# Kernel optimization log

Hardware: AMD Instinct MI355X
Metric: run time of the kernel (lower is better)

The kernel has to match this reference:

```python
import jax, jax.numpy as jnp
import numpy as np
from jax import lax

C, H, W = 256, 56, 56
KP, STRIDE = 9, 2
M_CH, D, T = 64, 128, 16
TOPK = 32
SIGMA, ALPHA, TAU, EPS = 3.0, 10.0, 10.0, 1e-6
B = 4
N = H * W
PAD = KP // 2


def _build_M_P(h, w, s):
    ys = np.arange(0, h, s)
    xs = np.arange(0, w, s)
    ny, nx = len(ys), len(xs)
    N_, K_ = h * w, ny * nx
    by, bx = np.meshgrid(np.arange(h, dtype=np.float32), np.arange(w, dtype=np.float32), indexing='ij')
    bx = bx.reshape(-1)
    by = by.reshape(-1)
    fx, fy = bx / float(s), by / float(s)
    x0 = np.floor(fx).astype(np.int64)
    y0 = np.floor(fy).astype(np.int64)
    x0c = np.clip(x0, 0, nx - 1)
    x1c = np.clip(x0 + 1, 0, nx - 1)
    y0c = np.clip(y0, 0, ny - 1)
    y1c = np.clip(y0 + 1, 0, ny - 1)
    wx = fx - x0
    wy = fy - y0
    Mm = np.zeros((N_, K_), dtype=np.float32)
    rows = np.arange(N_)
    Mm[rows, y0c * nx + x0c] += (1 - wx) * (1 - wy)
    Mm[rows, y0c * nx + x1c] += wx * (1 - wy)
    Mm[rows, y1c * nx + x0c] += (1 - wx) * wy
    Mm[rows, y1c * nx + x1c] += wx * wy
    rs = Mm.sum(1, keepdims=True)
    rs[rs == 0] = 1.0
    Mm = Mm / rs
    P = np.stack([bx, by], axis=-1).astype(np.float32)  # (N,2) (x,y)
    return Mm, P


def _forward(feature_map, A_bank, pw_w, pw_b, proj_w, proj_b, r, M, P):
    def make_grid(A):  # affine_grid, align_corners=False
        xs = (2.0 * jnp.arange(W, dtype=jnp.float32) + 1.0) / W - 1.0
        ys = (2.0 * jnp.arange(H, dtype=jnp.float32) + 1.0) / H - 1.0
        gy, gx = jnp.meshgrid(ys, xs, indexing='ij')
        base = jnp.stack([gx, gy, jnp.ones_like(gx)], axis=-1)  # (H,W,3)
        return base @ A.T  # (H,W,2) normalized (x,y)

    def grid_sample(grid):  # bilinear, border padding, align_corners=False
        ix = ((grid[..., 0] + 1.0) * W - 1.0) / 2.0
        iy = ((grid[..., 1] + 1.0) * H - 1.0) / 2.0
        x0 = jnp.floor(ix)
        y0 = jnp.floor(iy)
        wx = ix - x0
        wy = iy - y0
        x0c = jnp.clip(x0, 0, W - 1).astype(jnp.int32)
        x1c = jnp.clip(x0 + 1, 0, W - 1).astype(jnp.int32)
        y0c = jnp.clip(y0, 0, H - 1).astype(jnp.int32)
        y1c = jnp.clip(y0 + 1, 0, H - 1).astype(jnp.int32)
        fm = feature_map.reshape(B, C, H * W)
        def g(yc, xc):
            return fm[:, :, (yc * W + xc).reshape(-1)].reshape(B, C, H, W)
        return (g(y0c, x0c) * (1 - wx) * (1 - wy) + g(y0c, x1c) * wx * (1 - wy)
                + g(y1c, x0c) * (1 - wx) * wy + g(y1c, x1c) * wx * wy)

    grids = jax.vmap(make_grid)(A_bank)          # (T,H,W,2)
    warped = jax.vmap(grid_sample)(grids)        # (T,B,C,H,W)

    # unfold(k,pad,stride) -> 1x1 conv -> spatial mean  ==  zero-padded avg-pool then linear
    pm = lax.reduce_window(warped, 0.0, lax.add,
                           (1, 1, 1, KP, KP), (1, 1, 1, STRIDE, STRIDE),
                           [(0, 0), (0, 0), (0, 0), (PAD, PAD), (PAD, PAD)]) / (KP * KP)
    Tn, Bn, Cn, Kh, Kw = pm.shape
    K = Kh * Kw
    pm = pm.reshape(Tn, Bn, Cn, K).transpose(0, 1, 3, 2)  # (T,B,K,C)
    x = pm @ pw_w.T + pw_b                                 # (T,B,K,m)
    z = x @ proj_w.T + proj_b                              # (T,B,K,d)
    z = z / jnp.maximum(jnp.linalg.norm(z, axis=-1, keepdims=True), EPS)
    Z = z.transpose(1, 0, 2, 3)                            # (B,T,K,d)

    s = jnp.einsum('btkd,d->btk', Z, r)
    wgt = jax.nn.softmax(TAU * s, axis=1)[..., None]
    g_emb = jnp.sum(wgt * Z, axis=1)                       # (B,K,d)

    E = jnp.einsum('nk,bkd->bnd', M, g_emb)
    E = E / jnp.maximum(jnp.linalg.norm(E, axis=-1, keepdims=True), EPS)

    d2 = jnp.sum((P[:, None, :] - P[None, :, :]) ** 2, axis=-1)  # (N,N)
    G = 1.0 - jnp.exp(-d2 / (2.0 * SIGMA ** 2))
    Saff = jnp.einsum('bnd,bmd->bnm', E, E) * G

    vals, idx = lax.top_k(Saff, TOPK)
    bidx = jnp.arange(B)[:, None, None]
    nidx = jnp.arange(N)[None, :, None]
    S_sp = jnp.zeros_like(Saff).at[bidx, nidx, idx].set(vals)
    A0 = jax.nn.softmax(ALPHA * S_sp, axis=-1) * jax.nn.softmax(ALPHA * S_sp, axis=-2)
    return E, A0


def setup_inputs() -> dict:
    key = jax.random.key(0)
    ks = jax.random.split(key, 6)
    feature_map = jax.random.normal(ks[0], (B, C, H, W), jnp.float32)
    ident = jnp.broadcast_to(jnp.array([[1.0, 0.0, 0.0], [0.0, 1.0, 0.0]], jnp.float32), (T, 2, 3))
    A_bank = ident + 0.1 * jax.random.normal(ks[1], (T, 2, 3), jnp.float32)
    pw_w = jax.random.normal(ks[2], (M_CH, C), jnp.float32) / np.sqrt(C).astype(np.float32)
    pw_b = jnp.zeros((M_CH,), jnp.float32)
    proj_w = jax.random.normal(ks[3], (D, M_CH), jnp.float32) / np.sqrt(M_CH).astype(np.float32)
    proj_b = jnp.zeros((D,), jnp.float32)
    r = 0.01 * jax.random.normal(ks[4], (D,), jnp.float32)
    Mnp, Pnp = _build_M_P(H, W, STRIDE)
    return {'feature_map': feature_map, 'A_bank': A_bank, 'pw_w': pw_w, 'pw_b': pw_b,
            'proj_w': proj_w, 'proj_b': proj_b, 'r': r,
            'M': jnp.asarray(Mnp), 'P': jnp.asarray(Pnp)}


def reference(feature_map, A_bank, pw_w, pw_b, proj_w, proj_b, r, M, P):
    return _forward(feature_map, A_bank, pw_w, pw_b, proj_w, proj_b, r, M, P)
```

## Files before the change

kernel.cpp:

```cpp
#include <hip/hip_runtime.h>
#include <hip/hip_bf16.h>
#include <hip/hip_fp16.h>

#define Hh 56
#define Ww 56
#define Cc 256
#define Tt 16
#define Bb 4
#define Nn 3136
#define Kk 784
#define KX 28
#define Dd 128
#define Mc 64
#define NTOP 32

typedef __attribute__((ext_vector_type(8))) _Float16 f16x8;
typedef __attribute__((ext_vector_type(4))) float f32x4;

__global__ __launch_bounds__(128) void k_wc(
    const float* __restrict__ pw_w, const float* __restrict__ pw_b,
    const float* __restrict__ proj_w, const float* __restrict__ proj_b,
    float* __restrict__ wct, float* __restrict__ bc) {
  int c = blockIdx.x;
  int d = threadIdx.x;
  float acc = 0.f;
  for (int m = 0; m < Mc; ++m) acc += proj_w[d * Mc + m] * pw_w[m * Cc + c];
  wct[c * Dd + d] = acc;
  if (c == 0) {
    float bb = proj_b[d];
    for (int m = 0; m < Mc; ++m) bb += proj_w[d * Mc + m] * pw_b[m];
    bc[d] = bb;
  }
}

__global__ __launch_bounds__(256) void k_mix(
    const float* __restrict__ fm, const float* __restrict__ wct, float* __restrict__ y) {
  int blk = blockIdx.x;
  int b = blk / 112;
  int n0 = (blk % 112) * 28;
  int tid = threadIdx.x;
  int d = tid & 127;
  int ng = tid >> 7;
  __shared__ float fm_s[64 * 28];
  __shared__ float wc_s[64 * Dd];
  float acc[14];
#pragma unroll
  for (int j = 0; j < 14; ++j) acc[j] = 0.f;
  const float* fb = fm + (size_t)b * Cc * Nn;
  for (int c0 = 0; c0 < Cc; c0 += 64) {
    for (int i = tid; i < 64 * 28; i += 256) {
      int c = i / 28, kx = i - c * 28;
      fm_s[i] = fb[(size_t)(c0 + c) * Nn + n0 + kx];
    }
    for (int i = tid; i < 64 * Dd; i += 256) wc_s[i] = wct[c0 * Dd + i];
    __syncthreads();
    for (int c = 0; c < 64; ++c) {
      float w = wc_s[c * Dd + d];
#pragma unroll
      for (int j = 0; j < 14; ++j) acc[j] += fm_s[c * 28 + ng * 14 + j] * w;
    }
    __syncthreads();
  }
  size_t base = (((size_t)b * 64 + (d >> 1)) * Nn + n0 + ng * 14) * 2 + (d & 1);
#pragma unroll
  for (int j = 0; j < 14; ++j) y[base + 2 * j] = acc[j];
}

__global__ __launch_bounds__(256) void k_fused_pool(
    const float* __restrict__ yraw, const float* __restrict__ Abank,
    const float* __restrict__ bc, float* __restrict__ zt) {
  const float2* y2 = reinterpret_cast<const float2*>(yraw);
  int idx = blockIdx.x;
  int b = idx & 3;
  int pg = (idx >> 2) & 31;
  int t = idx >> 7;
  __shared__ float2 wsm[3136];
  __shared__ float2 rowp[1568];
  int tid = threadIdx.x;
  const float* A = Abank + t * 6;
  float a00 = A[0], a01 = A[1], a02 = A[2], a10 = A[3], a11 = A[4], a12 = A[5];
  int off[13];
  float wxa[13], wya[13];
#pragma unroll
  for (int j = 0; j < 13; ++j) {
    int e = tid + 256 * j;
    if (e < 3136) {
      int h = e / 56, w = e - h * 56;
      float gx = (2.0f * w + 1.0f) / 56.0f - 1.0f;
      float gy = (2.0f * h + 1.0f) / 56.0f - 1.0f;
      float u = a00 * gx + a01 * gy + a02;
      float v = a10 * gx + a11 * gy + a12;
      float ix = ((u + 1.0f) * 56.0f - 1.0f) * 0.5f;
      float iy = ((v + 1.0f) * 56.0f - 1.0f) * 0.5f;
      float x0f = floorf(ix), y0f = floorf(iy);
      wxa[j] = ix - x0f;
      wya[j] = iy - y0f;
      int x0 = (int)x0f, y0 = (int)y0f;
      int x0c = min(max(x0, 0), 55), x1c = min(max(x0 + 1, 0), 55);
      int y0c = min(max(y0, 0), 55), y1c = min(max(y0 + 1, 0), 55);
      off[j] = (y0c * 56 + x0c) | ((x1c - x0c) << 12) | ((y1c - y0c) << 13);
    }
  }
  for (int pp = 0; pp < 2; ++pp) {
    int dp = pg * 2 + pp;
    const float2* fc = y2 + ((size_t)b * 64 + dp) * Nn;
    float b0 = bc[dp * 2], b1 = bc[dp * 2 + 1];
#pragma unroll
    for (int j = 0; j < 13; ++j) {
      int e = tid + 256 * j;
      if (e < 3136) {
        int pk = off[j];
        int base = pk & 4095;
        int dx = (pk >> 12) & 1;
        int dyy = (pk & (1 << 13)) ? 56 : 0;
        float2 v00 = fc[base], v01 = fc[base + dx];
        float2 v10 = fc[base + dyy], v11 = fc[base + dyy + dx];
        float wx = wxa[j], wy = wya[j];
        float tx = v00.x + wx * (v01.x - v00.x);
        float bx = v10.x + wx * (v11.x - v10.x);
        float ty = v00.y + wx * (v01.y - v00.y);
        float by = v10.y + wx * (v11.y - v10.y);
        float2 o;
        o.x = tx + wy * (bx - tx);
        o.y = ty + wy * (by - ty);
        wsm[e] = o;
      }
    }
    __syncthreads();
    for (int e = tid; e < 1568; e += 256) {
      int h = e / 28, kx = e - h * 28;
      int xs = 2 * kx - 4;
      int lo = max(xs, 0), hi = min(xs + 8, 55);
      float sx = 0.f, sy = 0.f;
      const float2* wr = wsm + h * 56;
      for (int x = lo; x <= hi; ++x) { float2 v = wr[x]; sx += v.x; sy += v.y; }
      float2 o; o.x = sx; o.y = sy;
      rowp[e] = o;
    }
    __syncthreads();
    float* zo0 = zt + ((size_t)(t * Bb + b) * Dd + dp * 2) * Kk;
    float* zo1 = zo0 + Kk;
    for (int e = tid; e < 784; e += 256) {
      int ky = e / 28, kx = e - ky * 28;
      int ys = 2 * ky - 4;
      int lo = max(ys, 0), hi = min(ys + 8, 55);
      float sx = 0.f, sy = 0.f;
      for (int h = lo; h <= hi; ++h) { float2 rv = rowp[h * 28 + kx]; sx += rv.x; sy += rv.y; }
      zo0[e] = sx * (1.0f / 81.0f) + b0;
      zo1[e] = sy * (1.0f / 81.0f) + b1;
    }
    __syncthreads();
  }
}

__global__ __launch_bounds__(256) void k_znorm(
    const float* __restrict__ zt, const float* __restrict__ r,
    float* __restrict__ z, float* __restrict__ s_arr) {
  int tb = blockIdx.x / 14;
  int k0 = (blockIdx.x % 14) * 56;
  int tid = threadIdx.x;
  __shared__ float ls[56 * 129];
  const float* zb = zt + (size_t)tb * Dd * Kk + k0;
  for (int i = tid; i < Dd * 56; i += 256) {
    int d = i / 56, kk = i - d * 56;
    ls[kk * 129 + d] = zb[(size_t)d * Kk + kk];
  }
  int lane = tid & 63;
  int wv = tid >> 6;
  float r0 = r[lane], r1 = r[lane + 64];
  __syncthreads();
  for (int p = 0; p < 14; ++p) {
    int k = p * 4 + wv;
    float z0 = ls[k * 129 + lane];
    float z1 = ls[k * 129 + 64 + lane];
    float ss = z0 * z0 + z1 * z1;
    for (int off = 32; off; off >>= 1) ss += __shfl_xor(ss, off);
    float inv = 1.0f / fmaxf(sqrtf(ss), 1e-6f);
    z0 *= inv; z1 *= inv;
    float* zr = z + ((size_t)tb * Kk + k0 + k) * Dd;
    zr[lane] = z0;
    zr[lane + 64] = z1;
    float sd = z0 * r0 + z1 * r1;
    for (int off = 32; off; off >>= 1) sd += __shfl_xor(sd, off);
    if (lane == 0) s_arr[(size_t)tb * Kk + k0 + k] = sd;
  }
}

__global__ __launch_bounds__(128) void k_gemb(
    const float* __restrict__ z, const float* __restrict__ s_arr, float* __restrict__ g) {
  int blk = blockIdx.x;
  int b = blk / Kk, k = blk % Kk;
  int d = threadIdx.x;
  float sv[Tt];
  float mx = -3.4e38f;
#pragma unroll
  for (int t = 0; t < Tt; ++t) {
    sv[t] = s_arr[(t * Bb + b) * Kk + k];
    mx = fmaxf(mx, sv[t]);
  }
  float sum = 0.f;
#pragma unroll
  for (int t = 0; t < Tt; ++t) {
    sv[t] = expf(10.0f * (sv[t] - mx));
    sum += sv[t];
  }
  float isum = 1.0f / sum;
  float acc = 0.f;
#pragma unroll
  for (int t = 0; t < Tt; ++t)
    acc += sv[t] * isum * z[((size_t)(t * Bb + b) * Kk + k) * Dd + d];
  g[((size_t)b * Kk + k) * Dd + d] = acc;
}

__global__ __launch_bounds__(64) void k_E(
    const float* __restrict__ Mmat, const float* __restrict__ g,
    float* __restrict__ E, _Float16* __restrict__ E16) {
  int row = blockIdx.x;
  int b = row / Nn, n = row % Nn;
  int y = n / Ww, x = n % Ww;
  int x0 = x >> 1, y0 = y >> 1;
  int x1 = min(x0 + 1, 27), y1 = min(y0 + 1, 27);
  bool hx = (x1 != x0), hy = (y1 != y0);
  int k00 = y0 * 28 + x0, k01 = y0 * 28 + x1, k10 = y1 * 28 + x0, k11 = y1 * 28 + x1;
  const float* Mr = Mmat + (size_t)n * Kk;
  float m00 = Mr[k00];
  float m01 = hx ? Mr[k01] : 0.f;
  float m10 = hy ? Mr[k10] : 0.f;
  float m11 = (hx && hy) ? Mr[k11] : 0.f;
  const float* gb = g + (size_t)b * Kk * Dd;
  int lane = threadIdx.x;
  int l2 = lane + 64;
  float a0 = m00 * gb[k00 * Dd + lane] + m01 * gb[k01 * Dd + lane] +
             m10 * gb[k10 * Dd + lane] + m11 * gb[k11 * Dd + lane];
  float a1 = m00 * gb[k00 * Dd + l2] + m01 * gb[k01 * Dd + l2] +
             m10 * gb[k10 * Dd + l2] + m11 * gb[k11 * Dd + l2];
  float ss = a0 * a0 + a1 * a1;
  for (int off = 32; off; off >>= 1) ss += __shfl_xor(ss, off);
  float inv = 1.0f / fmaxf(sqrtf(ss), 1e-6f);
  float e0 = a0 * inv, e1 = a1 * inv;
  E[(size_t)row * Dd + lane] = e0;
  E[(size_t)row * Dd + l2] = e1;
  E16[(size_t)row * Dd + lane] = (_Float16)e0;
  E16[(size_t)row * Dd + l2] = (_Float16)e1;
}

__global__ __launch_bounds__(256) void k_saff(
    const _Float16* __restrict__ E16, __half* __restrict__ S) {
  int blk = blockIdx.x;
  int b = blk / 1225;
  int rem = blk % 1225;
  int ti0 = (int)((sqrtf(8.f * rem + 1.f) - 1.f) * 0.5f);
  while ((ti0 + 1) * (ti0 + 2) / 2 <= rem) ++ti0;
  while (ti0 * (ti0 + 1) / 2 > rem) --ti0;
  int tj0 = rem - ti0 * (ti0 + 1) / 2;
  int i0 = ti0 * 64, j0 = tj0 * 64;
  int wave = threadIdx.x >> 6, lane = threadIdx.x & 63;
  int wr = wave >> 1, wc = wave & 1;
  int lr = lane & 15, lk = lane >> 4;
  int ibase = i0 + wr * 32;
  int jbase = j0 + wc * 32;
  const _Float16* Eb = E16 + (size_t)b * Nn * Dd;
  __shared__ __half tile[64][66];
  f32x4 acc00 = {0.f, 0.f, 0.f, 0.f};
  f32x4 acc01 = acc00, acc10 = acc00, acc11 = acc00;
#pragma unroll
  for (int ks = 0; ks < 4; ++ks) {
    int ko = ks * 32 + lk * 8;
    f16x8 a0 = *reinterpret_cast<const f16x8*>(Eb + (size_t)(ibase + lr) * Dd + ko);
    f16x8 a1 = *reinterpret_cast<const f16x8*>(Eb + (size_t)(ibase + 16 + lr) * Dd + ko);
    f16x8 b0 = *reinterpret_cast<const f16x8*>(Eb + (size_t)(jbase + lr) * Dd + ko);
    f16x8 b1 = *reinterpret_cast<const f16x8*>(Eb + (size_t)(jbase + 16 + lr) * Dd + ko);
    acc00 = __builtin_amdgcn_mfma_f32_16x16x32_f16(a0, b0, acc00, 0, 0, 0);
    acc01 = __builtin_amdgcn_mfma_f32_16x16x32_f16(a0, b1, acc01, 0, 0, 0);
    acc10 = __builtin_amdgcn_mfma_f32_16x16x32_f16(a1, b0, acc10, 0, 0, 0);
    acc11 = __builtin_amdgcn_mfma_f32_16x16x32_f16(a1, b1, acc11, 0, 0, 0);
  }
  size_t ob = (size_t)b * Nn * Nn;
  int gj[2];
  float xj[2], yj[2];
#pragma unroll
  for (int tj = 0; tj < 2; ++tj) {
    gj[tj] = jbase + tj * 16 + lr;
    int yv = gj[tj] / 56;
    yj[tj] = (float)yv;
    xj[tj] = (float)(gj[tj] - yv * 56);
  }
  bool mirror = (i0 != j0);
#pragma unroll
  for (int ti = 0; ti < 2; ++ti) {
#pragma unroll
    for (int q = 0; q < 4; ++q) {
      int iloc = wr * 32 + ti * 16 + lk * 4 + q;
      int gi = i0 + iloc;
      int yiv = gi / 56;
      float yi = (float)yiv;
      float xi = (float)(gi - yiv * 56);
#pragma unroll
      for (int tj = 0; tj < 2; ++tj) {
        float a;
        if (ti == 0 && tj == 0) a = acc00[q];
        else if (ti == 0 && tj == 1) a = acc01[q];
        else if (ti == 1 && tj == 0) a = acc10[q];
        else a = acc11[q];
        float dx = xi - xj[tj];
        float dy = yi - yj[tj];
        float gg = 1.0f - __expf(-(dx * dx + dy * dy) * (1.0f / 18.0f));
        __half hv = __float2half(a * gg);
        S[ob + (size_t)gi * Nn + gj[tj]] = hv;
        int jloc = wc * 32 + tj * 16 + lr;
        tile[jloc][iloc] = hv;
      }
    }
  }
  if (mirror) {
    __syncthreads();
    for (int e = threadIdx.x; e < 64 * 32; e += 256) {
      int row = e >> 5, c2 = e & 31;
      unsigned v = *reinterpret_cast<const unsigned*>(&tile[row][c2 * 2]);
      *reinterpret_cast<unsigned*>(&S[ob + (size_t)(j0 + row) * Nn + i0 + c2 * 2]) = v;
    }
  }
}

__global__ __launch_bounds__(256) void k_topk(
    const __half* __restrict__ S16, const float* __restrict__ E,
    const float* __restrict__ P, float* __restrict__ topv, int* __restrict__ topi,
    float* __restrict__ dr, float* __restrict__ dc) {
  int row = blockIdx.x;
  int b = row / Nn, irow = row % Nn;
  int tid = threadIdx.x;
  const unsigned* Sr = reinterpret_cast<const unsigned*>(S16 + (size_t)row * Nn);
  __shared__ unsigned hist[256 * 8];
  __shared__ unsigned scan_s[256];
  __shared__ unsigned bcast[2];
  __shared__ unsigned sel_eq, sel_slot;
  __shared__ int sel_idx[NTOP];
  __shared__ float drow_s;
  unsigned pk[7];
#pragma unroll
  for (int j = 0; j < 7; ++j) {
    int c2 = tid + 256 * j;
    unsigned u = (c2 < Nn / 2) ? Sr[c2] : 0u;
    unsigned h0 = u & 0xFFFFu, h1 = u >> 16;
    unsigned k0 = h0 ^ ((h0 & 0x8000u) ? 0xFFFFu : 0x8000u);
    unsigned k1 = h1 ^ ((h1 & 0x8000u) ? 0xFFFFu : 0x8000u);
    if (c2 >= Nn / 2) { k0 = 0u; k1 = 0u; }
    pk[j] = k0 | (k1 << 16);
  }
  if (tid == 0) { sel_eq = 0; sel_slot = 0; drow_s = 0.f; }
  unsigned prefix = 0;
  unsigned k = NTOP;
  for (int pass = 0; pass < 2; ++pass) {
    int shift = 8 - 8 * pass;
    unsigned pmask = pass ? 0xFF00u : 0u;
#pragma unroll
    for (int i = 0; i < 8; ++i) hist[tid * 8 + i] = 0;
    __syncthreads();
#pragma unroll
    for (int j = 0; j < 7; ++j) {
      unsigned k0 = pk[j] & 0xFFFFu, k1 = pk[j] >> 16;
      if ((k0 & pmask) == (prefix & pmask))
        atomicAdd(&hist[((k0 >> shift) & 255u) * 8 + (tid & 7)], 1u);
      if ((k1 & pmask) == (prefix & pmask))
        atomicAdd(&hist[((k1 >> shift) & 255u) * 8 + (tid & 7)], 1u);
    }
    __syncthreads();
    unsigned cnt = 0;
#pragma unroll
    for (int i = 0; i < 8; ++i) cnt += hist[tid * 8 + i];
    unsigned run = cnt;
    scan_s[tid] = run;
    for (int st = 1; st < 256; st <<= 1) {
      __syncthreads();
      unsigned add = (tid + st < 256) ? scan_s[tid + st] : 0u;
      __syncthreads();
      run += add;
      scan_s[tid] = run;
    }
    unsigned incl = run;
    unsigned excl = incl - cnt;
    if (excl < k && k <= incl) {
      bcast[0] = prefix | ((unsigned)tid << shift);
      bcast[1] = k - excl;
    }
    __syncthreads();
    prefix = bcast[0];
    k = bcast[1];
    __syncthreads();
  }
  unsigned T = prefix;
#pragma unroll
  for (int j = 0; j < 7; ++j) {
    int c2 = tid + 256 * j;
    if (c2 < Nn / 2) {
      unsigned k0 = pk[j] & 0xFFFFu, k1 = pk[j] >> 16;
      bool take0 = (k0 > T) || (k0 == T && atomicAdd(&sel_eq, 1u) < k);
      if (take0) { unsigned slot = atomicAdd(&sel_slot, 1u); sel_idx[slot] = 2 * c2; }
      bool take1 = (k1 > T) || (k1 == T && atomicAdd(&sel_eq, 1u) < k);
      if (take1) { unsigned slot = atomicAdd(&sel_slot, 1u); sel_idx[slot] = 2 * c2 + 1; }
    }
  }
  __syncthreads();
  int sel = tid >> 3, part = tid & 7;
  int col = sel_idx[sel];
  const float* Ei = E + ((size_t)b * Nn + irow) * Dd;
  const float* Ej = E + ((size_t)b * Nn + col) * Dd;
  float v = 0.f;
#pragma unroll
  for (int d0 = 0; d0 < 16; ++d0) {
    int d = part * 16 + d0;
    v += Ei[d] * Ej[d];
  }
  v += __shfl_xor(v, 1);
  v += __shfl_xor(v, 2);
  v += __shfl_xor(v, 4);
  if (part == 0) {
    float dx = P[irow * 2] - P[col * 2];
    float dy = P[irow * 2 + 1] - P[col * 2 + 1];
    float gg = 1.0f - __expf(-(dx * dx + dy * dy) * (1.0f / 18.0f));
    v *= gg;
    topv[(size_t)row * NTOP + sel] = v;
    topi[(size_t)row * NTOP + sel] = col;
    float e = __expf(10.f * v);
    atomicAdd(&dc[b * Nn + col], e - 1.f);
    atomicAdd(&drow_s, e);
  }
  __syncthreads();
  if (tid == 0) dr[row] = (float)(Nn - NTOP) + drow_s;
}

__global__ void k_dcinit(float* __restrict__ dc) {
  int i = blockIdx.x * 256 + threadIdx.x;
  if (i < Bb * Nn) dc[i] = (float)Nn;
}

__global__ void k_inv(float* __restrict__ dr, float* __restrict__ dc) {
  int i = blockIdx.x * 256 + threadIdx.x;
  if (i < Bb * Nn) {
    dr[i] = 1.0f / dr[i];
    dc[i] = 1.0f / dc[i];
  }
}

__global__ __launch_bounds__(256) void k_basefix(
    const float* __restrict__ invdr, const float* __restrict__ invdc,
    const float* __restrict__ topv, const int* __restrict__ topi,
    float* __restrict__ A0) {
  int row = blockIdx.x;
  int b = row / Nn;
  float idr = invdr[row];
  const float4* dc4 = reinterpret_cast<const float4*>(invdc + b * Nn);
  float4* out4 = reinterpret_cast<float4*>(A0 + (size_t)row * Nn);
  for (int j = threadIdx.x; j < Nn / 4; j += 256) {
    float4 c = dc4[j];
    float4 o = {idr * c.x, idr * c.y, idr * c.z, idr * c.w};
    out4[j] = o;
  }
  __syncthreads();
  if (threadIdx.x < NTOP) {
    int gidx = row * NTOP + threadIdx.x;
    int col = topi[gidx];
    float e = __expf(10.f * topv[gidx]);
    A0[(size_t)row * Nn + col] = e * e * idr * invdc[b * Nn + col];
  }
}

extern "C" void kernel_launch(void* const* d_in, const int* in_sizes, int n_in,
                              void* d_out, int out_size, void* d_ws, size_t ws_size,
                              hipStream_t stream) {
  const float* fm     = (const float*)d_in[0];
  const float* Abank  = (const float*)d_in[1];
  const float* pw_w   = (const float*)d_in[2];
  const float* pw_b   = (const float*)d_in[3];
  const float* proj_w = (const float*)d_in[4];
  const float* proj_b = (const float*)d_in[5];
  const float* r      = (const float*)d_in[6];
  const float* Mmat   = (const float*)d_in[7];
  const float* P      = (const float*)d_in[8];
  float* out = (float*)d_out;
  float* E  = out;
  float* A0 = out + (size_t)Bb * Nn * Dd;
  __half* S16 = (__half*)A0;

  float* ws = (float*)d_ws;
  float* y     = ws;
  float* zt    = ws + 1605632;
  float* z     = ws + 8028160;
  float* wct   = ws + 14450688;
  float* bcv   = ws + 14483456;
  float* s_arr = ws + 14483584;
  float* g     = ws + 14533760;
  float* topv  = ws + 14935168;
  int*   topi  = (int*)(ws + 15336576);
  float* dr    = ws + 15737984;
  float* dc    = ws + 15750528;
  _Float16* E16 = (_Float16*)(ws + 15763072);

  hipLaunchKernelGGL(k_wc, dim3(Cc), dim3(128), 0, stream, pw_w, pw_b, proj_w, proj_b, wct, bcv);
  hipLaunchKernelGGL(k_mix, dim3(448), dim3(256), 0, stream, fm, wct, y);
  hipLaunchKernelGGL(k_fused_pool, dim3(2048), dim3(256), 0, stream, y, Abank, bcv, zt);
  hipLaunchKernelGGL(k_znorm, dim3(64 * 14), dim3(256), 0, stream, zt, r, z, s_arr);
  hipLaunchKernelGGL(k_gemb, dim3(Bb * Kk), dim3(128), 0, stream, z, s_arr, g);
  hipLaunchKernelGGL(k_E, dim3(Bb * Nn), dim3(64), 0, stream, Mmat, g, E, E16);
  hipLaunchKernelGGL(k_saff, dim3(Bb * 1225), dim3(256), 0, stream, E16, S16);
  hipLaunchKernelGGL(k_dcinit, dim3(49), dim3(256), 0, stream, dc);
  hipLaunchKernelGGL(k_topk, dim3(Bb * Nn), dim3(256), 0, stream, S16, E, P, topv, topi, dr, dc);
  hipLaunchKernelGGL(k_inv, dim3(49), dim3(256), 0, stream, dr, dc);
  hipLaunchKernelGGL(k_basefix, dim3(Bb * Nn), dim3(256), 0, stream, dr, dc, topv, topi, A0);
}
```

Before: 436.4 us.

## Precompute sampling coords, widen mix tile, pack E rows, wave-scan topk histogram

Moves the affine-grid coordinate and bilinear-weight computation into a small precompute kernel, so the pool blocks load packed offsets and weights instead of recomputing them per block. Retiles the channel-mix GEMM to 32 pixels per block and reads shared memory with float4 loads. Packs two rows per block in k_E to reduce tiny 64-thread blocks. Replaces the shared-memory Hillis-Steele scan in top-k with wavefront shuffle scans plus a cross-wave sum, cutting many __syncthreads per pass. These add an extra launch and workspace buffers.

```diff
diff --git a/kernel.cpp b/kernel.cpp
--- a/kernel.cpp
+++ b/kernel.cpp
@@ -33,42 +33,73 @@
   }
 }
 
+__global__ __launch_bounds__(256) void k_coords(
+    const float* __restrict__ Abank, unsigned* __restrict__ offo,
+    float2* __restrict__ wo) {
+  int t = blockIdx.x;
+  const float* A = Abank + t * 6;
+  float a00 = A[0], a01 = A[1], a02 = A[2], a10 = A[3], a11 = A[4], a12 = A[5];
+  for (int e = threadIdx.x; e < Nn; e += 256) {
+    int h = e / 56, w = e - h * 56;
+    float gx = (2.0f * w + 1.0f) / 56.0f - 1.0f;
+    float gy = (2.0f * h + 1.0f) / 56.0f - 1.0f;
+    float u = a00 * gx + a01 * gy + a02;
+    float v = a10 * gx + a11 * gy + a12;
+    float ix = ((u + 1.0f) * 56.0f - 1.0f) * 0.5f;
+    float iy = ((v + 1.0f) * 56.0f - 1.0f) * 0.5f;
+    float x0f = floorf(ix), y0f = floorf(iy);
+    int x0 = (int)x0f, y0 = (int)y0f;
+    int x0c = min(max(x0, 0), 55), x1c = min(max(x0 + 1, 0), 55);
+    int y0c = min(max(y0, 0), 55), y1c = min(max(y0 + 1, 0), 55);
+    offo[t * Nn + e] = (y0c * 56 + x0c) | ((x1c - x0c) << 12) | ((y1c - y0c) << 13);
+    float2 wv2;
+    wv2.x = ix - x0f;
+    wv2.y = iy - y0f;
+    wo[t * Nn + e] = wv2;
+  }
+}
+
 __global__ __launch_bounds__(256) void k_mix(
     const float* __restrict__ fm, const float* __restrict__ wct, float* __restrict__ y) {
   int blk = blockIdx.x;
-  int b = blk / 112;
-  int n0 = (blk % 112) * 28;
+  int b = blk / 98;
+  int n0 = (blk % 98) * 32;
   int tid = threadIdx.x;
   int d = tid & 127;
   int ng = tid >> 7;
-  __shared__ float fm_s[64 * 28];
+  __shared__ __align__(16) float fm_s[64][32];
   __shared__ float wc_s[64 * Dd];
-  float acc[14];
-#pragma unroll
-  for (int j = 0; j < 14; ++j) acc[j] = 0.f;
+  float acc[16];
+#pragma unroll
+  for (int j = 0; j < 16; ++j) acc[j] = 0.f;
   const float* fb = fm + (size_t)b * Cc * Nn;
   for (int c0 = 0; c0 < Cc; c0 += 64) {
-    for (int i = tid; i < 64 * 28; i += 256) {
-      int c = i / 28, kx = i - c * 28;
-      fm_s[i] = fb[(size_t)(c0 + c) * Nn + n0 + kx];
+    for (int i = tid; i < 64 * 32; i += 256) {
+      int c = i >> 5, kx = i & 31;
+      fm_s[c][kx] = fb[(size_t)(c0 + c) * Nn + n0 + kx];
     }
     for (int i = tid; i < 64 * Dd; i += 256) wc_s[i] = wct[c0 * Dd + i];
     __syncthreads();
     for (int c = 0; c < 64; ++c) {
       float w = wc_s[c * Dd + d];
-#pragma unroll
-      for (int j = 0; j < 14; ++j) acc[j] += fm_s[c * 28 + ng * 14 + j] * w;
-    }
-    __syncthreads();
-  }
-  size_t base = (((size_t)b * 64 + (d >> 1)) * Nn + n0 + ng * 14) * 2 + (d & 1);
-#pragma unroll
-  for (int j = 0; j < 14; ++j) y[base + 2 * j] = acc[j];
+      const float4* fr = reinterpret_cast<const float4*>(&fm_s[c][ng * 16]);
+      float4 f0 = fr[0], f1 = fr[1], f2 = fr[2], f3 = fr[3];
+      acc[0]  += f0.x * w; acc[1]  += f0.y * w; acc[2]  += f0.z * w; acc[3]  += f0.w * w;
+      acc[4]  += f1.x * w; acc[5]  += f1.y * w; acc[6]  += f1.z * w; acc[7]  += f1.w * w;
+      acc[8]  += f2.x * w; acc[9]  += f2.y * w; acc[10] += f2.z * w; acc[11] += f2.w * w;
+      acc[12] += f3.x * w; acc[13] += f3.y * w; acc[14] += f3.z * w; acc[15] += f3.w * w;
+    }
+    __syncthreads();
+  }
+  size_t base = (((size_t)b * 64 + (d >> 1)) * Nn + n0 + ng * 16) * 2 + (d & 1);
+#pragma unroll
+  for (int j = 0; j < 16; ++j) y[base + 2 * j] = acc[j];
 }
 
 __global__ __launch_bounds__(256) void k_fused_pool(
-    const float* __restrict__ yraw, const float* __restrict__ Abank,
-    const float* __restrict__ bc, float* __restrict__ zt) {
+    const float* __restrict__ yraw, const unsigned* __restrict__ offo,
+    const float2* __restrict__ wo, const float* __restrict__ bc,
+    float* __restrict__ zt) {
   const float2* y2 = reinterpret_cast<const float2*>(yraw);
   int idx = blockIdx.x;
   int b = idx & 3;
@@ -77,28 +108,16 @@
   __shared__ float2 wsm[3136];
   __shared__ float2 rowp[1568];
   int tid = threadIdx.x;
-  const float* A = Abank + t * 6;
-  float a00 = A[0], a01 = A[1], a02 = A[2], a10 = A[3], a11 = A[4], a12 = A[5];
-  int off[13];
-  float wxa[13], wya[13];
+  const unsigned* offp = offo + t * Nn;
+  const float2* wp = wo + t * Nn;
+  unsigned off[13];
+  float2 wv[13];
 #pragma unroll
   for (int j = 0; j < 13; ++j) {
     int e = tid + 256 * j;
     if (e < 3136) {
-      int h = e / 56, w = e - h * 56;
-      float gx = (2.0f * w + 1.0f) / 56.0f - 1.0f;
-      float gy = (2.0f * h + 1.0f) / 56.0f - 1.0f;
-      float u = a00 * gx + a01 * gy + a02;
-      float v = a10 * gx + a11 * gy + a12;
-      float ix = ((u + 1.0f) * 56.0f - 1.0f) * 0.5f;
-      float iy = ((v + 1.0f) * 56.0f - 1.0f) * 0.5f;
-      float x0f = floorf(ix), y0f = floorf(iy);
-      wxa[j] = ix - x0f;
-      wya[j] = iy - y0f;
-      int x0 = (int)x0f, y0 = (int)y0f;
-      int x0c = min(max(x0, 0), 55), x1c = min(max(x0 + 1, 0), 55);
-      int y0c = min(max(y0, 0), 55), y1c = min(max(y0 + 1, 0), 55);
-      off[j] = (y0c * 56 + x0c) | ((x1c - x0c) << 12) | ((y1c - y0c) << 13);
+      off[j] = offp[e];
+      wv[j] = wp[e];
     }
   }
   for (int pp = 0; pp < 2; ++pp) {
@@ -109,13 +128,13 @@
     for (int j = 0; j < 13; ++j) {
       int e = tid + 256 * j;
       if (e < 3136) {
-        int pk = off[j];
+        unsigned pk = off[j];
         int base = pk & 4095;
         int dx = (pk >> 12) & 1;
-        int dyy = (pk & (1 << 13)) ? 56 : 0;
+        int dyy = (pk & (1u << 13)) ? 56 : 0;
         float2 v00 = fc[base], v01 = fc[base + dx];
         float2 v10 = fc[base + dyy], v11 = fc[base + dyy + dx];
-        float wx = wxa[j], wy = wya[j];
+        float wx = wv[j].x, wy = wv[j].y;
         float tx = v00.x + wx * (v01.x - v00.x);
         float bx = v10.x + wx * (v11.x - v10.x);
         float ty = v00.y + wx * (v01.y - v00.y);
@@ -166,11 +185,11 @@
     ls[kk * 129 + d] = zb[(size_t)d * Kk + kk];
   }
   int lane = tid & 63;
-  int wv = tid >> 6;
+  int wvv = tid >> 6;
   float r0 = r[lane], r1 = r[lane + 64];
   __syncthreads();
   for (int p = 0; p < 14; ++p) {
-    int k = p * 4 + wv;
+    int k = p * 4 + wvv;
     float z0 = ls[k * 129 + lane];
     float z1 = ls[k * 129 + 64 + lane];
     float ss = z0 * z0 + z1 * z1;
@@ -212,10 +231,10 @@
   g[((size_t)b * Kk + k) * Dd + d] = acc;
 }
 
-__global__ __launch_bounds__(64) void k_E(
+__global__ __launch_bounds__(128) void k_E(
     const float* __restrict__ Mmat, const float* __restrict__ g,
     float* __restrict__ E, _Float16* __restrict__ E16) {
-  int row = blockIdx.x;
+  int row = blockIdx.x * 2 + (threadIdx.x >> 6);
   int b = row / Nn, n = row % Nn;
   int y = n / Ww, x = n % Ww;
   int x0 = x >> 1, y0 = y >> 1;
@@ -228,7 +247,7 @@
   float m10 = hy ? Mr[k10] : 0.f;
   float m11 = (hx && hy) ? Mr[k11] : 0.f;
   const float* gb = g + (size_t)b * Kk * Dd;
-  int lane = threadIdx.x;
+  int lane = threadIdx.x & 63;
   int l2 = lane + 64;
   float a0 = m00 * gb[k00 * Dd + lane] + m01 * gb[k01 * Dd + lane] +
              m10 * gb[k10 * Dd + lane] + m11 * gb[k11 * Dd + lane];
@@ -331,7 +350,7 @@
   int tid = threadIdx.x;
   const unsigned* Sr = reinterpret_cast<const unsigned*>(S16 + (size_t)row * Nn);
   __shared__ unsigned hist[256 * 8];
-  __shared__ unsigned scan_s[256];
+  __shared__ unsigned wtot[4];
   __shared__ unsigned bcast[2];
   __shared__ unsigned sel_eq, sel_slot;
   __shared__ int sel_idx[NTOP];
@@ -348,6 +367,7 @@
     pk[j] = k0 | (k1 << 16);
   }
   if (tid == 0) { sel_eq = 0; sel_slot = 0; drow_s = 0.f; }
+  int lane = tid & 63, wvq = tid >> 6;
   unsigned prefix = 0;
   unsigned k = NTOP;
   for (int pass = 0; pass < 2; ++pass) {
@@ -369,15 +389,16 @@
 #pragma unroll
     for (int i = 0; i < 8; ++i) cnt += hist[tid * 8 + i];
     unsigned run = cnt;
-    scan_s[tid] = run;
-    for (int st = 1; st < 256; st <<= 1) {
-      __syncthreads();
-      unsigned add = (tid + st < 256) ? scan_s[tid + st] : 0u;
-      __syncthreads();
-      run += add;
-      scan_s[tid] = run;
-    }
-    unsigned incl = run;
+#pragma unroll
+    for (int off2 = 1; off2 < 64; off2 <<= 1) {
+      unsigned v = __shfl_down(run, off2);
+      if (lane + off2 < 64) run += v;
+    }
+    if (lane == 0) wtot[wvq] = run;
+    __syncthreads();
+    unsigned hi = 0;
+    for (int w2 = wvq + 1; w2 < 4; ++w2) hi += wtot[w2];
+    unsigned incl = run + hi;
     unsigned excl = incl - cnt;
     if (excl < k && k <= incl) {
       bcast[0] = prefix | ((unsigned)tid << shift);
@@ -495,13 +516,16 @@
   float* dr    = ws + 15737984;
   float* dc    = ws + 15750528;
   _Float16* E16 = (_Float16*)(ws + 15763072);
+  unsigned* offo = (unsigned*)(ws + 16565888);
+  float2*   wo   = (float2*)(ws + 16616064);
 
   hipLaunchKernelGGL(k_wc, dim3(Cc), dim3(128), 0, stream, pw_w, pw_b, proj_w, proj_b, wct, bcv);
-  hipLaunchKernelGGL(k_mix, dim3(448), dim3(256), 0, stream, fm, wct, y);
-  hipLaunchKernelGGL(k_fused_pool, dim3(2048), dim3(256), 0, stream, y, Abank, bcv, zt);
+  hipLaunchKernelGGL(k_coords, dim3(Tt), dim3(256), 0, stream, Abank, offo, wo);
+  hipLaunchKernelGGL(k_mix, dim3(392), dim3(256), 0, stream, fm, wct, y);
+  hipLaunchKernelGGL(k_fused_pool, dim3(2048), dim3(256), 0, stream, y, offo, wo, bcv, zt);
   hipLaunchKernelGGL(k_znorm, dim3(64 * 14), dim3(256), 0, stream, zt, r, z, s_arr);
   hipLaunchKernelGGL(k_gemb, dim3(Bb * Kk), dim3(128), 0, stream, z, s_arr, g);
-  hipLaunchKernelGGL(k_E, dim3(Bb * Nn), dim3(64), 0, stream, Mmat, g, E, E16);
+  hipLaunchKernelGGL(k_E, dim3(Bb * Nn / 2), dim3(128), 0, stream, Mmat, g, E, E16);
   hipLaunchKernelGGL(k_saff, dim3(Bb * 1225), dim3(256), 0, stream, E16, S16);
   hipLaunchKernelGGL(k_dcinit, dim3(49), dim3(256), 0, stream, dc);
   hipLaunchKernelGGL(k_topk, dim3(Bb * Nn), dim3(256), 0, stream, S16, E, P, topv, topi, dr, dc);
```

Measured after the change: 427.0 us. -2.1%, faster.
